# Optimization experiments

Hardware: AMD Instinct MI355X
Metric: run time of the kernel (lower is better)

## Reference

```python
import jax, jax.numpy as jnp
import numpy as np

FEATS = 768
HEAD = 12


def _phi(t):
    # elu feature map + 1 (guarantees positivity)
    return jax.nn.elu(t) + 1.0


def setup_inputs() -> dict:
    key = jax.random.key(0)
    ks = jax.random.split(key, 9)
    f = FEATS
    s = 1.0 / np.sqrt(f)
    x = jax.random.normal(ks[0], (4, 4096, f), dtype=jnp.float32)
    # weights stored as [in, out] so projection is x @ W + b
    Wq = jax.random.normal(ks[1], (f, f), dtype=jnp.float32) * s
    bq = jax.random.normal(ks[2], (f,), dtype=jnp.float32) * 0.01
    Wk = jax.random.normal(ks[3], (f, f), dtype=jnp.float32) * s
    bk = jax.random.normal(ks[4], (f,), dtype=jnp.float32) * 0.01
    Wv = jax.random.normal(ks[5], (f, f), dtype=jnp.float32) * s
    bv = jax.random.normal(ks[6], (f,), dtype=jnp.float32) * 0.01
    Wo = jax.random.normal(ks[7], (f, f), dtype=jnp.float32) * s
    bo = jax.random.normal(ks[8], (f,), dtype=jnp.float32) * 0.01
    return {"x": x, "Wq": Wq, "bq": bq, "Wk": Wk, "bk": bk,
            "Wv": Wv, "bv": bv, "Wo": Wo, "bo": bo}


def reference(x, Wq, bq, Wk, bk, Wv, bv, Wo, bo):
    b, n, f = x.shape
    h = HEAD
    d = f // h
    # project and split heads: [b, h, n, d]
    def heads(t):
        return t.reshape(b, n, h, d).transpose(0, 2, 1, 3)
    q = _phi(heads(x @ Wq + bq))
    k = _phi(heads(x @ Wk + bk))
    v = heads(x @ Wv + bv)
    # kv summary: [b, h, d, d] (sum over sequence)
    kv = jnp.einsum('bhnd,bhne->bhde', k, v)
    # normalizer: z[b,h,l] = 1 / (q[b,h,l,:] . sum_n k[b,h,n,:])  (no eps, as in source)
    ksum = k.sum(axis=2)                      # [b, h, d]
    z = 1.0 / jnp.einsum('bhld,bhd->bhl', q, ksum)  # [b, h, n]
    num = jnp.einsum('bhld,bhde->bhle', q, kv)      # [b, h, n, d]
    normed = num * z[..., None]                     # [b, h, n, d]
    out = normed.transpose(0, 2, 1, 3).reshape(b, n, f)  # [b, n, f]
    return out @ Wo + bo  # dropout p=0.0 -> identity
```

## Files before the change

### kernel.cpp

```cpp
#include <hip/hip_runtime.h>
#include <cstdint>
#include <cstddef>

#define DEVI __device__ __forceinline__

typedef short    shortx8 __attribute__((ext_vector_type(8)));
typedef short    shortx4 __attribute__((ext_vector_type(4)));
typedef short    shortx2 __attribute__((ext_vector_type(2)));
typedef __bf16   bf16x8  __attribute__((ext_vector_type(8)));
typedef float    floatx4 __attribute__((ext_vector_type(4)));

DEVI unsigned short f2b(float f) {
    union { float f; unsigned u; } a; a.f = f;
    unsigned r = a.u + 0x7fffu + ((a.u >> 16) & 1u);
    return (unsigned short)(r >> 16);
}
DEVI float b2f(unsigned short u) {
    union { unsigned u; float f; } a; a.u = ((unsigned)u) << 16;
    return a.f;
}

DEVI floatx4 mfma_bf16(bf16x8 a, bf16x8 b, floatx4 c) {
    return __builtin_amdgcn_mfma_f32_16x16x32_bf16(a, b, c, 0, 0, 0);
}

DEVI void glds16(const ushort* g, ushort* l) {
    __builtin_amdgcn_global_load_lds(
        (const __attribute__((address_space(1))) void*)g,
        (__attribute__((address_space(3))) void*)l, 16, 0, 0);
}

__global__ void k_prep(const float* __restrict__ x, ushort* __restrict__ xb,
                       const float* __restrict__ Wq, const float* __restrict__ Wk,
                       const float* __restrict__ Wv, const float* __restrict__ Wo,
                       ushort* __restrict__ Wt, ushort* __restrict__ Wot,
                       const float* __restrict__ bq, const float* __restrict__ bk,
                       const float* __restrict__ bv, float* __restrict__ bqkv) {
    __shared__ float tile[64][65];
    const int bid = blockIdx.x, t = threadIdx.x;
    if (bid < 6144) {
        size_t i = ((size_t)bid * 256 + t) * 8;
        float4 v0 = *(const float4*)(x + i);
        float4 v1 = *(const float4*)(x + i + 4);
        shortx8 o;
        o[0] = (short)f2b(v0.x); o[1] = (short)f2b(v0.y);
        o[2] = (short)f2b(v0.z); o[3] = (short)f2b(v0.w);
        o[4] = (short)f2b(v1.x); o[5] = (short)f2b(v1.y);
        o[6] = (short)f2b(v1.z); o[7] = (short)f2b(v1.w);
        *(shortx8*)(xb + i) = o;
    } else if (bid < 6720) {
        int pid = bid - 6144;
        int zi = pid / 144, rem = pid % 144;
        const float* W = (zi == 0) ? Wq : (zi == 1) ? Wk : (zi == 2) ? Wv : Wo;
        const int i0 = (rem / 12) * 64, j0 = (rem % 12) * 64;
        const int c = t & 63, r4 = t >> 6;
        for (int rr = r4; rr < 64; rr += 4)
            tile[rr][c] = W[(size_t)(i0 + rr) * 768 + j0 + c];
        __syncthreads();
        ushort* dst = (zi < 3) ? (Wt + (size_t)(zi * 768) * 768) : Wot;
        for (int jj = r4; jj < 64; jj += 4)
            dst[(size_t)(j0 + jj) * 768 + i0 + c] = f2b(tile[c][jj]);
    } else {
        int j = (bid - 6720) * 256 + t;
        if (j < 2304) {
            const float* src = (j < 768) ? bq : (j < 1536) ? bk : bv;
            bqkv[j] = src[j % 768];
        }
    }
}

template <int MODE>
__global__ __launch_bounds__(256, 4) void k_gemm(
    const ushort* __restrict__ A, const ushort* __restrict__ Bt,
    const float* __restrict__ bias, void* __restrict__ Cout, int Ncols) {
    constexpr int K = 768;
    constexpr int GY = (MODE == 0) ? 18 : 6;
    constexpr int NWG = 128 * GY;
    __shared__ ushort As[128 * 64];
    __shared__ ushort Bs[128 * 64];

    const int lin  = blockIdx.y * 128 + blockIdx.x;
    const int wg   = (lin & 7) * (NWG / 8) + (lin >> 3);
    const int band = wg / (8 * GY);
    const int rem  = wg % (8 * GY);
    const int m0 = (band * 8 + (rem & 7)) * 128;
    const int n0 = (rem >> 3) * 128;

    const int tid = threadIdx.x;
    const int w = tid >> 6, lane = tid & 63;

    const int lr = lane >> 3;
    const int lc = ((lane & 7) ^ lr) * 8;
    const ushort* aBase = A  + (size_t)(m0 + w * 32 + lr) * K + lc;
    const ushort* bBase = Bt + (size_t)(n0 + w * 32 + lr) * K + lc;
    ushort* aL = As + (w * 32) * 64;
    ushort* bL = Bs + (w * 32) * 64;

    const int rBase = (w >> 1) * 64;
    const int nBase = (w & 1) * 64;
    const int fr = lane & 15;
    const int q4 = lane >> 4;

    floatx4 acc[4][4] = {};

    for (int k0 = 0; k0 < K; k0 += 64) {
#pragma unroll
        for (int i = 0; i < 4; ++i) glds16(aBase + i * (8 * K) + k0, aL + i * (8 * 64));
#pragma unroll
        for (int i = 0; i < 4; ++i) glds16(bBase + i * (8 * K) + k0, bL + i * (8 * 64));
        __syncthreads();
#pragma unroll
        for (int kc = 0; kc < 2; ++kc) {
            const int off = ((kc * 4 + q4) ^ (fr & 7)) * 8;
            bf16x8 af[4], bf[4];
#pragma unroll
            for (int rt = 0; rt < 4; ++rt)
                af[rt] = *(const bf16x8*)(As + (rBase + rt * 16 + fr) * 64 + off);
#pragma unroll
            for (int nt = 0; nt < 4; ++nt)
                bf[nt] = *(const bf16x8*)(Bs + (nBase + nt * 16 + fr) * 64 + off);
#pragma unroll
            for (int rt = 0; rt < 4; ++rt)
#pragma unroll
                for (int nt = 0; nt < 4; ++nt)
                    acc[rt][nt] = mfma_bf16(af[rt], bf[nt], acc[rt][nt]);
        }
        __syncthreads();
    }

#pragma unroll
    for (int rt = 0; rt < 4; ++rt) {
#pragma unroll
        for (int nt = 0; nt < 4; ++nt) {
#pragma unroll
            for (int r = 0; r < 4; ++r) {
                int m = m0 + rBase + rt * 16 + q4 * 4 + r;
                int n = n0 + nBase + nt * 16 + fr;
                float v = acc[rt][nt][r] + bias[n];
                if (MODE == 0) {
                    if (n < 1536) v = (v > 0.f) ? (v + 1.f) : __expf(v);
                    ((ushort*)Cout)[(size_t)m * Ncols + n] = f2b(v);
                } else {
                    ((float*)Cout)[(size_t)m * Ncols + n] = v;
                }
            }
        }
    }
}

#define KV_LOAD(rr, r)  do {                                          \
    const ushort* kp = base + (size_t)((rr) * 64 + n_ld) * 2304;      \
    r[0] = *(const shortx8*)(kp);                                     \
    r[1] = *(const shortx8*)(kp + 8);                                 \
    r[2] = *(const shortx8*)(kp + 768);                               \
    r[3] = *(const shortx8*)(kp + 776); } while (0)

#define KV_STORE(buf, r) do {                                         \
    union { shortx8 v8; shortx2 v2[4]; } u0, u1, u2, u3;              \
    u0.v8 = r[0]; u1.v8 = r[1]; u2.v8 = r[2]; u3.v8 = r[3];           \
    ushort* kd = kS[buf] + n_ld * 70 + c16;                           \
    ushort* vd = vS[buf] + n_ld * 70 + c16;                           \
    _Pragma("unroll")                                                 \
    for (int i = 0; i < 4; ++i) {                                     \
        *(shortx2*)(kd + 2 * i)     = u0.v2[i];                       \
        *(shortx2*)(kd + 8 + 2 * i) = u1.v2[i];                       \
        *(shortx2*)(vd + 2 * i)     = u2.v2[i];                       \
        *(shortx2*)(vd + 8 + 2 * i) = u3.v2[i]; } } while (0)

__global__ __launch_bounds__(256) void k_kv(const ushort* __restrict__ QKV,
                                            float* __restrict__ kvp) {
    const int bh = blockIdx.x, s = blockIdx.y;
    const int bb = bh / 12, head = bh % 12;
    __shared__ ushort kS[2][64 * 70];
    __shared__ ushort vS[2][64 * 70];
    const int t = threadIdx.x, w = t >> 6, lane = t & 63;
    const int fr = lane & 15, fk = (lane >> 4) * 8;

    floatx4 acc[5] = {};
    const int n_ld = t >> 2, c16 = (t & 3) * 16;
    const ushort* base = QKV + (size_t)(bb * 4096 + s * 256) * 2304 + 768 + head * 64 + c16;

    union { bf16x8 v; ushort u[8]; } ones;
    {
        ushort ov = (fr == 0) ? (ushort)0x3F80 : (ushort)0;
#pragma unroll
        for (int i = 0; i < 8; ++i) ones.u[i] = ov;
    }

    shortx8 rA[4], rB[4];
    KV_LOAD(0, rA);
    KV_STORE(0, rA);

#pragma unroll
    for (int rr = 0; rr < 4; ++rr) {
        __syncthreads();
        if (rr == 0)      KV_LOAD(1, rB);
        else if (rr == 1) KV_LOAD(2, rA);
        else if (rr == 2) KV_LOAD(3, rB);
        const int buf = rr & 1;
#pragma unroll
        for (int kl = 0; kl < 64; kl += 32) {
            union { bf16x8 v; ushort u[8]; } bfr, afr[4];
#pragma unroll
            for (int i = 0; i < 8; ++i) {
                int n = kl + fk + i;
                bfr.u[i] = kS[buf][n * 70 + w * 16 + fr];
#pragma unroll
                for (int mt = 0; mt < 4; ++mt)
                    afr[mt].u[i] = vS[buf][n * 70 + mt * 16 + fr];
            }
#pragma unroll
            for (int mt = 0; mt < 4; ++mt)
                acc[mt] = mfma_bf16(afr[mt].v, bfr.v, acc[mt]);
            acc[4] = mfma_bf16(ones.v, bfr.v, acc[4]);
        }
        if (rr == 0)      KV_STORE(1, rB);
        else if (rr == 1) KV_STORE(0, rA);
        else if (rr == 2) KV_STORE(1, rB);
    }

    float* dst = kvp + ((size_t)bh * 16 + s) * (65 * 64);
#pragma unroll
    for (int mt = 0; mt < 4; ++mt)
#pragma unroll
        for (int r = 0; r < 4; ++r)
            dst[(mt * 16 + (lane >> 4) * 4 + r) * 64 + w * 16 + fr] = acc[mt][r];
    if (lane < 16) dst[64 * 64 + w * 16 + lane] = acc[4][0];
}

__global__ void k_kvred(const float* __restrict__ kvp, ushort* __restrict__ kvb) {
    int t4 = (blockIdx.x * 256 + threadIdx.x) * 4;
    int bh = t4 / 4160, rem = t4 % 4160;
    const float* p = kvp + (size_t)bh * 16 * 4160 + rem;
    float4 sum = {0.f, 0.f, 0.f, 0.f};
    for (int i = 0; i < 16; ++i) {
        float4 a = *(const float4*)(p + (size_t)i * 4160);
        sum.x += a.x; sum.y += a.y; sum.z += a.z; sum.w += a.w;
    }
    shortx4 o;
    o[0] = (short)f2b(sum.x); o[1] = (short)f2b(sum.y);
    o[2] = (short)f2b(sum.z); o[3] = (short)f2b(sum.w);
    *(shortx4*)(kvb + t4) = o;
}

__global__ __launch_bounds__(256) void k_num(const ushort* __restrict__ QKV,
                                             const ushort* __restrict__ kvb,
                                             ushort* __restrict__ normed) {
    const int bh = blockIdx.x, l0 = blockIdx.y * 128;
    const int bb = bh / 12, head = bh % 12;
    __shared__ ushort qsh[128 * 72];
    __shared__ ushort kvT[80 * 72];
    __shared__ float dnm[128];
    const int t = threadIdx.x, w = t >> 6, lane = t & 63;

    {
        const ushort* kvbb = kvb + (size_t)bh * 4160;
        int c8 = (t & 7) * 8;
        for (int r0 = (t >> 3); r0 < 65; r0 += 32)
            *(shortx8*)(kvT + r0 * 72 + c8) = *(const shortx8*)(kvbb + r0 * 64 + c8);
    }
    for (int idx = t; idx < 15 * 72; idx += 256) kvT[65 * 72 + idx] = 0;

    const ushort* qg = QKV + (size_t)(bb * 4096 + l0) * 2304 + head * 64;
    {
        int row = t >> 3, c8 = (t & 7) * 8;
#pragma unroll
        for (int i = 0; i < 4; ++i) {
            shortx8 v = *(const shortx8*)(qg + (size_t)(i * 32 + row) * 2304 + c8);
            *(shortx8*)(qsh + (i * 32 + row) * 72 + c8) = v;
        }
    }
    __syncthreads();

    const int fr = lane & 15, fk = (lane >> 4) * 8;
    floatx4 acc[2][5] = {};
#pragma unroll
    for (int kc = 0; kc < 2; ++kc) {
        bf16x8 a[2], b[5];
#pragma unroll
        for (int rt = 0; rt < 2; ++rt)
            a[rt] = *(const bf16x8*)(qsh + (w * 32 + rt * 16 + fr) * 72 + kc * 32 + fk);
#pragma unroll
        for (int nt = 0; nt < 5; ++nt)
            b[nt] = *(const bf16x8*)(kvT + (nt * 16 + fr) * 72 + kc * 32 + fk);
#pragma unroll
        for (int rt = 0; rt < 2; ++rt)
#pragma unroll
            for (int nt = 0; nt < 5; ++nt)
                acc[rt][nt] = mfma_bf16(a[rt], b[nt], acc[rt][nt]);
    }
    if (fr == 0) {
#pragma unroll
        for (int rt = 0; rt < 2; ++rt)
#pragma unroll
            for (int r = 0; r < 4; ++r)
                dnm[w * 32 + rt * 16 + (lane >> 4) * 4 + r] = acc[rt][4][r];
    }
    __syncthreads();
#pragma unroll
    for (int rt = 0; rt < 2; ++rt) {
#pragma unroll
        for (int r = 0; r < 4; ++r) {
            int ml = w * 32 + rt * 16 + (lane >> 4) * 4 + r;
            float z = 1.f / dnm[ml];
            size_t base = (size_t)(bb * 4096 + l0 + ml) * 768 + head * 64;
#pragma unroll
            for (int nt = 0; nt < 4; ++nt)
                normed[base + nt * 16 + fr] = f2b(acc[rt][nt][r] * z);
        }
    }
}

extern "C" void kernel_launch(void* const* d_in, const int* in_sizes, int n_in,
                              void* d_out, int out_size, void* d_ws, size_t ws_size,
                              hipStream_t stream) {
    const float* x  = (const float*)d_in[0];
    const float* Wq = (const float*)d_in[1];
    const float* bq = (const float*)d_in[2];
    const float* Wk = (const float*)d_in[3];
    const float* bk = (const float*)d_in[4];
    const float* Wv = (const float*)d_in[5];
    const float* bv = (const float*)d_in[6];
    const float* Wo = (const float*)d_in[7];
    const float* bo = (const float*)d_in[8];

    char* ws = (char*)d_ws;
    ushort* Xb   = (ushort*)(ws);
    ushort* Wt   = (ushort*)(ws + 25165824);
    ushort* Wot  = (ushort*)(ws + 28704768);
    float*  bqkv = (float*)(ws + 29884416);
    ushort* QKV  = (ushort*)(ws + 29893632);
    ushort* kvb  = (ushort*)(ws + 111780864);
    float*  kvp  = (float*)(ws);
    ushort* normed = Xb;

    k_prep <<<dim3(6729),      256, 0, stream>>>(x, Xb, Wq, Wk, Wv, Wo, Wt, Wot,
                                                 bq, bk, bv, bqkv);
    k_gemm<0><<<dim3(128, 18), 256, 0, stream>>>(Xb, Wt, bqkv, (void*)QKV, 2304);
    k_kv   <<<dim3(48, 16),    256, 0, stream>>>(QKV, kvp);
    k_kvred<<<dim3(195),       256, 0, stream>>>(kvp, kvb);
    k_num  <<<dim3(48, 32),    256, 0, stream>>>(QKV, kvb, normed);
    k_gemm<1><<<dim3(128, 6),  256, 0, stream>>>(normed, Wot, bo, d_out, 768);
}
```

Before: 230.9 us.

## Fuse normalized attention numerator into output projection GEMM

Replaces the separate numerator kernel and output GEMM with one kernel. For each head it computes q·kv and the normalizer into shared memory, then immediately multiplies by the matching Wo slice, accumulating the projection. This removes the round trip of the normalized activations through global memory and one launch. In exchange, the q·kv work and Q loads are repeated for each of the six output column tiles, and each head step adds several block barriers with no load/compute overlap.

```diff
diff --git a/kernel.cpp b/kernel.cpp
--- a/kernel.cpp
+++ b/kernel.cpp
@@ -243,70 +243,125 @@
     *(shortx4*)(kvb + t4) = o;
 }
 
-__global__ __launch_bounds__(256) void k_num(const ushort* __restrict__ QKV,
-                                             const ushort* __restrict__ kvb,
-                                             ushort* __restrict__ normed) {
-    const int bh = blockIdx.x, l0 = blockIdx.y * 128;
-    const int bb = bh / 12, head = bh % 12;
+__global__ __launch_bounds__(256, 3) void k_fng(
+    const ushort* __restrict__ QKV, const ushort* __restrict__ kvb,
+    const ushort* __restrict__ Wot, const float* __restrict__ bias,
+    float* __restrict__ Cout) {
+    constexpr int GY = 6;
+    constexpr int NWG = 128 * GY;
     __shared__ ushort qsh[128 * 72];
     __shared__ ushort kvT[80 * 72];
+    __shared__ ushort Bs[128 * 64];
     __shared__ float dnm[128];
+
+    const int lin  = blockIdx.y * 128 + blockIdx.x;
+    const int wg   = (lin & 7) * (NWG / 8) + (lin >> 3);
+    const int band = wg / (8 * GY);
+    const int rem  = wg % (8 * GY);
+    const int m0 = (band * 8 + (rem & 7)) * 128;
+    const int n0 = (rem >> 3) * 128;
+
     const int t = threadIdx.x, w = t >> 6, lane = t & 63;
-
-    {
-        const ushort* kvbb = kvb + (size_t)bh * 4160;
-        int c8 = (t & 7) * 8;
-        for (int r0 = (t >> 3); r0 < 65; r0 += 32)
-            *(shortx8*)(kvT + r0 * 72 + c8) = *(const shortx8*)(kvbb + r0 * 64 + c8);
-    }
+    const int fr = lane & 15, q4 = lane >> 4, fk = q4 * 8;
+    const int lr = lane >> 3, lc = ((lane & 7) ^ lr) * 8;
+    const int rBase = (w >> 1) * 64, nBase = (w & 1) * 64;
+
+    const ushort* bgBase = Wot + (size_t)(n0 + w * 32 + lr) * 768 + lc;
+    ushort* bL = Bs + (w * 32) * 64;
+    const int srow = t >> 3, sc8 = (t & 7) * 8;
+    const ushort* kvbase = kvb + (size_t)(m0 >> 12) * 12 * 4160;
+    const ushort* qgBase = QKV + (size_t)m0 * 2304;
+
     for (int idx = t; idx < 15 * 72; idx += 256) kvT[65 * 72 + idx] = 0;
 
-    const ushort* qg = QKV + (size_t)(bb * 4096 + l0) * 2304 + head * 64;
-    {
-        int row = t >> 3, c8 = (t & 7) * 8;
-#pragma unroll
-        for (int i = 0; i < 4; ++i) {
-            shortx8 v = *(const shortx8*)(qg + (size_t)(i * 32 + row) * 2304 + c8);
-            *(shortx8*)(qsh + (i * 32 + row) * 72 + c8) = v;
-        }
-    }
-    __syncthreads();
-
-    const int fr = lane & 15, fk = (lane >> 4) * 8;
-    floatx4 acc[2][5] = {};
-#pragma unroll
-    for (int kc = 0; kc < 2; ++kc) {
-        bf16x8 a[2], b[5];
-#pragma unroll
-        for (int rt = 0; rt < 2; ++rt)
-            a[rt] = *(const bf16x8*)(qsh + (w * 32 + rt * 16 + fr) * 72 + kc * 32 + fk);
-#pragma unroll
-        for (int nt = 0; nt < 5; ++nt)
-            b[nt] = *(const bf16x8*)(kvT + (nt * 16 + fr) * 72 + kc * 32 + fk);
-#pragma unroll
-        for (int rt = 0; rt < 2; ++rt)
+    floatx4 acc[4][4] = {};
+
+    for (int h = 0; h < 12; ++h) {
+#pragma unroll
+        for (int i = 0; i < 4; ++i)
+            glds16(bgBase + i * (8 * 768) + h * 64, bL + i * 512);
+        {
+            const ushort* kvbb = kvbase + h * 4160;
+            for (int r0 = srow; r0 < 65; r0 += 32)
+                *(shortx8*)(kvT + r0 * 72 + sc8) = *(const shortx8*)(kvbb + r0 * 64 + sc8);
+        }
+        {
+            const ushort* qg = qgBase + h * 64;
+#pragma unroll
+            for (int i = 0; i < 4; ++i) {
+                shortx8 v = *(const shortx8*)(qg + (size_t)(i * 32 + srow) * 2304 + sc8);
+                *(shortx8*)(qsh + (i * 32 + srow) * 72 + sc8) = v;
+            }
+        }
+        __syncthreads();
+
+        floatx4 acc2[2][5] = {};
+#pragma unroll
+        for (int kc = 0; kc < 2; ++kc) {
+            bf16x8 a[2], b[5];
+#pragma unroll
+            for (int rt = 0; rt < 2; ++rt)
+                a[rt] = *(const bf16x8*)(qsh + (w * 32 + rt * 16 + fr) * 72 + kc * 32 + fk);
 #pragma unroll
             for (int nt = 0; nt < 5; ++nt)
-                acc[rt][nt] = mfma_bf16(a[rt], b[nt], acc[rt][nt]);
-    }
-    if (fr == 0) {
-#pragma unroll
-        for (int rt = 0; rt < 2; ++rt)
-#pragma unroll
-            for (int r = 0; r < 4; ++r)
-                dnm[w * 32 + rt * 16 + (lane >> 4) * 4 + r] = acc[rt][4][r];
-    }
-    __syncthreads();
-#pragma unroll
-    for (int rt = 0; rt < 2; ++rt) {
-#pragma unroll
-        for (int r = 0; r < 4; ++r) {
-            int ml = w * 32 + rt * 16 + (lane >> 4) * 4 + r;
-            float z = 1.f / dnm[ml];
-            size_t base = (size_t)(bb * 4096 + l0 + ml) * 768 + head * 64;
+                b[nt] = *(const bf16x8*)(kvT + (nt * 16 + fr) * 72 + kc * 32 + fk);
+#pragma unroll
+            for (int rt = 0; rt < 2; ++rt)
+#pragma unroll
+                for (int nt = 0; nt < 5; ++nt)
+                    acc2[rt][nt] = mfma_bf16(a[rt], b[nt], acc2[rt][nt]);
+        }
+        if (fr == 0) {
+#pragma unroll
+            for (int rt = 0; rt < 2; ++rt)
+#pragma unroll
+                for (int r = 0; r < 4; ++r)
+                    dnm[w * 32 + rt * 16 + q4 * 4 + r] = acc2[rt][4][r];
+        }
+        __syncthreads();
+
+#pragma unroll
+        for (int rt = 0; rt < 2; ++rt) {
+#pragma unroll
+            for (int r = 0; r < 4; ++r) {
+                int ml = w * 32 + rt * 16 + q4 * 4 + r;
+                float z = 1.f / dnm[ml];
+#pragma unroll
+                for (int nt = 0; nt < 4; ++nt)
+                    qsh[ml * 72 + nt * 16 + fr] = f2b(acc2[rt][nt][r] * z);
+            }
+        }
+        __syncthreads();
+
+#pragma unroll
+        for (int kc = 0; kc < 2; ++kc) {
+            const int off = ((kc * 4 + q4) ^ (fr & 7)) * 8;
+            bf16x8 af[4], bf[4];
+#pragma unroll
+            for (int rt = 0; rt < 4; ++rt)
+                af[rt] = *(const bf16x8*)(qsh + (rBase + rt * 16 + fr) * 72 + kc * 32 + fk);
 #pragma unroll
             for (int nt = 0; nt < 4; ++nt)
-                normed[base + nt * 16 + fr] = f2b(acc[rt][nt][r] * z);
+                bf[nt] = *(const bf16x8*)(Bs + (nBase + nt * 16 + fr) * 64 + off);
+#pragma unroll
+            for (int rt = 0; rt < 4; ++rt)
+#pragma unroll
+                for (int nt = 0; nt < 4; ++nt)
+                    acc[rt][nt] = mfma_bf16(af[rt], bf[nt], acc[rt][nt]);
+        }
+        __syncthreads();
+    }
+
+#pragma unroll
+    for (int rt = 0; rt < 4; ++rt) {
+#pragma unroll
+        for (int nt = 0; nt < 4; ++nt) {
+#pragma unroll
+            for (int r = 0; r < 4; ++r) {
+                int m = m0 + rBase + rt * 16 + q4 * 4 + r;
+                int n = n0 + nBase + nt * 16 + fr;
+                Cout[(size_t)m * 768 + n] = acc[rt][nt][r] + bias[n];
+            }
         }
     }
 }
@@ -332,13 +387,11 @@
     ushort* QKV  = (ushort*)(ws + 29893632);
     ushort* kvb  = (ushort*)(ws + 111780864);
     float*  kvp  = (float*)(ws);
-    ushort* normed = Xb;
 
     k_prep <<<dim3(6729),      256, 0, stream>>>(x, Xb, Wq, Wk, Wv, Wo, Wt, Wot,
                                                  bq, bk, bv, bqkv);
     k_gemm<0><<<dim3(128, 18), 256, 0, stream>>>(Xb, Wt, bqkv, (void*)QKV, 2304);
     k_kv   <<<dim3(48, 16),    256, 0, stream>>>(QKV, kvp);
     k_kvred<<<dim3(195),       256, 0, stream>>>(kvp, kvb);
-    k_num  <<<dim3(48, 32),    256, 0, stream>>>(QKV, kvb, normed);
-    k_gemm<1><<<dim3(128, 6),  256, 0, stream>>>(normed, Wot, bo, d_out, 768);
-}
+    k_fng  <<<dim3(128, 6),    256, 0, stream>>>(QKV, kvb, Wot, bo, (float*)d_out);
+}
```

Result: slower. 251.2 us (+8.8%).
